# Kernel optimization log

Hardware: AMD Instinct MI355X
Metric: run time of the kernel (lower is better)

Reference implementation:

```python
import jax, jax.numpy as jnp
import numpy as np
import math

D = 768; H = 8; HD = D // H; T = 1024; V = 32000; M = 10
BLOCK = 128          # flex-attention block size (sliding_window_num_blocks granularity)
TAU = 1.0            # gumbel_temp
MAXC = 10            # max middle-block visits == scan length
EPS = 1e-6
IFP = 0.95           # initial_forward_prob

def rms(x):
    return x * jax.lax.rsqrt(jnp.mean(x * x, axis=-1, keepdims=True) + EPS)

def make_rope(t):
    # Rotary.__init__: dim//4 real inv freqs + dim//4 zeros -> cos/sin of shape [t, HD//2]
    inv = (1.0 / 1024) ** jnp.linspace(0.0, 1.0, HD // 4)
    inv = jnp.concatenate([inv, jnp.zeros(HD // 4)])
    th = jnp.arange(t, dtype=jnp.float32)[:, None] * inv[None, :]
    return jnp.cos(th), jnp.sin(th)

def rope(x, cos, sin):
    # x: [1,T,H,HD]
    c = cos[None, :, None, :]; s = sin[None, :, None, :]
    x1, x2 = jnp.split(x, 2, axis=-1)
    return jnp.concatenate([x1 * c + x2 * s, -x1 * s + x2 * c], axis=-1)

def attn(x, ve, wq, wk, wv, wo, lam, cos, sin, mask):
    q = (x @ wq.T).reshape(1, T, H, HD)
    k = (x @ wk.T).reshape(1, T, H, HD)
    v = (x @ wv.T).reshape(1, T, H, HD)
    if ve is not None:
        v = lam[0] * v + lam[1] * ve.reshape(1, T, H, HD)
    else:
        v = lam[0] * v
    q = rope(rms(q), cos, sin); k = rope(rms(k), cos, sin)
    sc = jnp.einsum('bthd,bshd->bhts', q, k) * (1.0 / math.sqrt(HD))
    sc = jnp.where(mask, sc, -1e30)
    y = jnp.einsum('bhts,bshd->bthd', jax.nn.softmax(sc, axis=-1), v).reshape(1, T, D)
    return y @ wo.T

def mlp(x, fc, pr):
    return jnp.square(jax.nn.relu(x @ fc.T)) @ pr.T

def fwd(tokens, embed_w, ve_w, lm_head_w,
        in_wq, in_wk, in_wv, in_wo, in_attn_lam, in_fc, in_pr, in_lam,
        mid_wq, mid_wk, mid_wv, mid_wo, mid_attn_lam, mid_fc, mid_pr, router_w, router_b,
        out_wq, out_wk, out_wv, out_wo, out_attn_lam, out_fc, out_pr, out_lam,
        gumbel_u, window_blocks, max_block_count):
    cos, sin = make_rope(T)
    qi = jnp.arange(T)
    mask = ((qi[:, None] >= qi[None, :]) &
            ((qi[:, None] // BLOCK - qi[None, :] // BLOCK) < window_blocks))[None, None]
    x = rms(embed_w[tokens][None])     # norm(embed(inputs))
    x0 = x
    ve = ve_w[tokens][None]            # X=1 value embedding, reused for output block
    # ---- input FixedBlock ----
    h = in_lam[0] * x + in_lam[1] * x0
    h = h + attn(rms(h), ve, in_wq, in_wk, in_wv, in_wo, in_attn_lam, cos, sin, mask)
    h = h + mlp(rms(h), in_fc, in_pr)
    # ---- middle routing loop (fixed-length scan, masked once exited) ----
    g = -jnp.log(-jnp.log(gumbel_u + 1e-10) + 1e-10)  # [MAXC, M+1] gumbel noise
    mbc = jnp.float32(max_block_count)
    def step(carry, gi):
        x, cur, done, cnt = carry
        y = x + attn(rms(x), None, mid_wq[cur], mid_wk[cur], mid_wv[cur], mid_wo[cur],
                     mid_attn_lam[cur], cos, sin, mask)
        y = y + mlp(rms(y), mid_fc[cur], mid_pr[cur])
        feat = jnp.concatenate([y.mean(axis=1), jnp.stack([cnt, mbc])[None]], axis=-1)  # [1, D+2]
        logits = feat @ router_w[cur].T + router_b[cur]                                  # [1, M+1]
        route = jax.nn.softmax((logits + gi[None]) / TAU, axis=-1)
        nxt = jnp.argmax(route[0]).astype(jnp.int32)
        new_cnt = cnt + 1.0
        exit_now = (nxt == M) | (new_cnt >= mbc)
        x = jnp.where(done, x, y)
        cnt = jnp.where(done, cnt, new_cnt)
        new_done = done | exit_now
        cur = jnp.where(new_done, cur, nxt)
        return (x, cur, new_done, cnt), None
    init = (h, jnp.int32(0), jnp.bool_(False), jnp.float32(0.0))
    (x, _, _, _), _ = jax.lax.scan(step, init, g)
    # ---- output FixedBlock ----
    y = out_lam[0] * x + out_lam[1] * x0
    y = y + attn(rms(y), ve, out_wq, out_wk, out_wv, out_wo, out_attn_lam, cos, sin, mask)
    y = y + mlp(rms(y), out_fc, out_pr)
    logits = rms(y) @ lm_head_w.T
    return 30.0 * jnp.tanh(logits / 30.0)

def setup_inputs() -> dict:
    key = jax.random.key(0)
    ks = iter(jax.random.split(key, 64))
    def w(*s, std=0.02):
        return (std * jax.random.normal(next(ks), s)).astype(jnp.float32)
    rb = np.full((M, M + 1), math.log((1.0 - IFP) / M), dtype=np.float32)
    for i in range(M):
        rb[i, min(i + 1, M)] = math.log(IFP)
    inp = {
        'tokens': jax.random.randint(next(ks), (T,), 0, V, dtype=jnp.int32),
        'embed_w': w(V, D), 've_w': w(V, D), 'lm_head_w': w(V, D),
        'in_wq': w(D, D), 'in_wk': w(D, D), 'in_wv': w(D, D), 'in_wo': w(D, D),
        'in_attn_lam': jnp.array([0.5, 0.5], jnp.float32),
        'in_fc': w(4 * D, D), 'in_pr': w(D, 4 * D),
        'in_lam': jnp.array([1.0, 0.0], jnp.float32),
        'mid_wq': w(M, D, D), 'mid_wk': w(M, D, D), 'mid_wv': w(M, D, D), 'mid_wo': w(M, D, D),
        'mid_attn_lam': jnp.tile(jnp.array([0.5, 0.5], jnp.float32), (M, 1)),
        'mid_fc': w(M, 4 * D, D), 'mid_pr': w(M, D, 4 * D),
        'router_w': w(M, M + 1, D + 2, std=0.001),
        'router_b': jnp.asarray(rb),
        'out_wq': w(D, D), 'out_wk': w(D, D), 'out_wv': w(D, D), 'out_wo': w(D, D),
        'out_attn_lam': jnp.array([0.5, 0.5], jnp.float32),
        'out_fc': w(4 * D, D), 'out_pr': w(D, 4 * D),
        'out_lam': jnp.array([1.0, 0.0], jnp.float32),
        'gumbel_u': jax.random.uniform(next(ks), (MAXC, M + 1), dtype=jnp.float32),
        'window_blocks': 4,
        'max_block_count': MAXC,
    }
    return inp

def reference(tokens, embed_w, ve_w, lm_head_w,
              in_wq, in_wk, in_wv, in_wo, in_attn_lam, in_fc, in_pr, in_lam,
              mid_wq, mid_wk, mid_wv, mid_wo, mid_attn_lam, mid_fc, mid_pr, router_w, router_b,
              out_wq, out_wk, out_wv, out_wo, out_attn_lam, out_fc, out_pr, out_lam,
              gumbel_u, window_blocks, max_block_count):
    return fwd(tokens, embed_w, ve_w, lm_head_w,
               in_wq, in_wk, in_wv, in_wo, in_attn_lam, in_fc, in_pr, in_lam,
               mid_wq, mid_wk, mid_wv, mid_wo, mid_attn_lam, mid_fc, mid_pr, router_w, router_b,
               out_wq, out_wk, out_wv, out_wo, out_attn_lam, out_fc, out_pr, out_lam,
               gumbel_u, window_blocks, max_block_count)
```

## Files before the change

### kernel.cpp

```cpp
#include <hip/hip_runtime.h>
#include <hip/hip_bf16.h>

namespace {

constexpr int cT   = 1024;
constexpr int cD   = 768;
constexpr int cH   = 8;
constexpr int cHD  = 96;
constexpr int cM   = 10;
constexpr int cDff = 3072;
constexpr int cV   = 32000;
constexpr int cTD  = cT * cD;
constexpr float cEps = 1e-6f;

constexpr long oWQ = 0;
constexpr long oWK = 589824;
constexpr long oWV = 2L * 589824;
constexpr long oWO = 3L * 589824;
constexpr long oFC = 4L * 589824;
constexpr long oPR = 4L * 589824 + 2359296;
constexpr long cWTOT = 4L * 589824 + 2L * 2359296;

typedef __attribute__((ext_vector_type(8))) short short8;
typedef __attribute__((ext_vector_type(4))) float f32x4;

__device__ inline short bf16r(float f) {
  union { float f; unsigned u; } x{f};
  unsigned r = (x.u + 0x7FFF + ((x.u >> 16) & 1)) >> 16;
  return (short)r;
}

__device__ inline float bf2f(short s) {
  union { unsigned u; float f; } x;
  x.u = ((unsigned)(unsigned short)s) << 16;
  return x.f;
}


__global__ void init_state_k(int* cur, int* done, float* cnt) {
  if (threadIdx.x == 0) { *cur = 0; *done = 0; *cnt = 0.0f; }
}

__global__ void rope_pre_k(float* __restrict__ cosb, float* __restrict__ sinb) {
  int idx = blockIdx.x * blockDim.x + threadIdx.x;
  if (idx >= cT * 48) return;
  int t = idx / 48, j = idx % 48;
  float th = 0.0f;
  if (j < 24) th = (float)t * powf(1.0f / 1024.0f, (float)j / 23.0f);
  cosb[idx] = cosf(th);
  sinb[idx] = sinf(th);
}

__global__ __launch_bounds__(256) void embed_rms_k(const int* __restrict__ tok,
    const float* __restrict__ ew, const float* __restrict__ vw,
    float* __restrict__ x0, float* __restrict__ ve) {
  int t = blockIdx.x;
  int tk = tok[t];
  const float* er = ew + (size_t)tk * cD;
  const float* vr = vw + (size_t)tk * cD;
  __shared__ float red[256];
  float s = 0.f;
  for (int d = threadIdx.x; d < cD; d += 256) { float e = er[d]; s += e * e; }
  red[threadIdx.x] = s; __syncthreads();
  for (int st = 128; st; st >>= 1) { if (threadIdx.x < st) red[threadIdx.x] += red[threadIdx.x + st]; __syncthreads(); }
  float sc = rsqrtf(red[0] / cD + cEps);
  for (int d = threadIdx.x; d < cD; d += 256) {
    x0[(size_t)t * cD + d] = er[d] * sc;
    ve[(size_t)t * cD + d] = vr[d];
  }
}

__global__ __launch_bounds__(256) void rms_rows_bf(const float* __restrict__ in,
    short* __restrict__ out, const int* done) {
  if (done && *done) return;
  int t = blockIdx.x;
  const float* r = in + (size_t)t * cD;
  __shared__ float red[256];
  float s = 0.f;
  for (int d = threadIdx.x; d < cD; d += 256) { float v = r[d]; s += v * v; }
  red[threadIdx.x] = s; __syncthreads();
  for (int st = 128; st; st >>= 1) { if (threadIdx.x < st) red[threadIdx.x] += red[threadIdx.x + st]; __syncthreads(); }
  float sc = rsqrtf(red[0] / cD + cEps);
  short* o = out + (size_t)t * cD;
  for (int d = threadIdx.x; d < cD; d += 256) o[d] = bf16r(r[d] * sc);
}

__global__ void axpy_lam_k(const float* __restrict__ lam, const float* __restrict__ a,
                           const float* __restrict__ b, float* __restrict__ o, int n) {
  int i = blockIdx.x * 256 + threadIdx.x;
  if (i < n) o[i] = lam[0] * a[i] + lam[1] * b[i];
}


__global__ __launch_bounds__(256) void convertw_k(const float* __restrict__ s0,
    const float* __restrict__ s1, const float* __restrict__ s2, const float* __restrict__ s3,
    const float* __restrict__ s4, const float* __restrict__ s5, short* __restrict__ dst,
    const int* __restrict__ cur, const int* __restrict__ done) {
  if (done && *done) return;
  long e = ((long)blockIdx.x * 256 + threadIdx.x) * 8;
  if (e >= cWTOT) return;
  long cu = cur ? (long)(*cur) : 0L;
  const float* src;
  if (e < oWK)      src = s0 + cu * 589824  + e;
  else if (e < oWV) src = s1 + cu * 589824  + (e - oWK);
  else if (e < oWO) src = s2 + cu * 589824  + (e - oWV);
  else if (e < oFC) src = s3 + cu * 589824  + (e - oWO);
  else if (e < oPR) src = s4 + cu * 2359296 + (e - oFC);
  else              src = s5 + cu * 2359296 + (e - oPR);
  float4 a0 = *(const float4*)src;
  float4 a1 = *(const float4*)(src + 4);
  short8 sv;
  sv[0]=bf16r(a0.x); sv[1]=bf16r(a0.y); sv[2]=bf16r(a0.z); sv[3]=bf16r(a0.w);
  sv[4]=bf16r(a1.x); sv[5]=bf16r(a1.y); sv[6]=bf16r(a1.z); sv[7]=bf16r(a1.w);
  *(short8*)(dst + e) = sv;
}

__global__ __launch_bounds__(256) void conv1_k(const float* __restrict__ src,
    short* __restrict__ dst, long nchunk) {
  long i = (long)blockIdx.x * 256 + threadIdx.x;
  if (i >= nchunk) return;
  long e = i * 8;
  float4 a0 = *(const float4*)(src + e);
  float4 a1 = *(const float4*)(src + e + 4);
  short8 sv;
  sv[0]=bf16r(a0.x); sv[1]=bf16r(a0.y); sv[2]=bf16r(a0.z); sv[3]=bf16r(a0.w);
  sv[4]=bf16r(a1.x); sv[5]=bf16r(a1.y); sv[6]=bf16r(a1.z); sv[7]=bf16r(a1.w);
  *(short8*)(dst + e) = sv;
}


__global__ __launch_bounds__(256) void qkv_k(const short* __restrict__ A,
    const short* __restrict__ Wb,
    short* __restrict__ qo, short* __restrict__ ko, short* __restrict__ vo,
    const int* __restrict__ done, const float* __restrict__ lamb,
    const int* __restrict__ cur, const float* __restrict__ vep,
    const float* __restrict__ cosb, const float* __restrict__ sinb) {
  if (done && *done) return;
  const int z = blockIdx.z;
  const short* W = Wb + (long)z * 589824L;
  const int h  = blockIdx.x;
  const int bm = blockIdx.y * 64;
  __shared__ short As[2][64][40];
  __shared__ short Bs[2][96][40];
  const int tid = threadIdx.x;
  const int w = tid >> 6, lane = tid & 63;
  const int fr = lane & 15, fg = lane >> 4;
  const int ar = tid >> 2, ac2 = (tid & 3) << 3;
  const int br1 = (256 + tid) >> 2, bc1 = ((256 + tid) & 3) << 3;

  short8 aN, bN0, bN1;
  aN  = *(const short8*)(A + (size_t)(bm + ar) * cD + ac2);
  bN0 = *(const short8*)(W + (size_t)(h * cHD + ar) * cD + ac2);
  if (tid < 128) bN1 = *(const short8*)(W + (size_t)(h * cHD + br1) * cD + bc1);
  *(short8*)&As[0][ar][ac2] = aN;
  *(short8*)&Bs[0][ar][ac2] = bN0;
  if (tid < 128) *(short8*)&Bs[0][br1][bc1] = bN1;
  __syncthreads();

  f32x4 acc[6] = {};
  int cb = 0;
  for (int kt = 0; kt < cD; kt += 32) {
    const int ktn = kt + 32;
    const bool hn = ktn < cD;
    if (hn) {
      aN  = *(const short8*)(A + (size_t)(bm + ar) * cD + ktn + ac2);
      bN0 = *(const short8*)(W + (size_t)(h * cHD + ar) * cD + ktn + ac2);
      if (tid < 128) bN1 = *(const short8*)(W + (size_t)(h * cHD + br1) * cD + ktn + bc1);
    }
    short8 af = *(const short8*)&As[cb][w * 16 + fr][fg * 8];
#pragma unroll
    for (int n = 0; n < 6; ++n) {
      short8 bf = *(const short8*)&Bs[cb][n * 16 + fr][fg * 8];
      acc[n] = __builtin_amdgcn_mfma_f32_16x16x32_bf16(af, bf, acc[n], 0, 0, 0);
    }
    if (hn) {
      *(short8*)&As[cb ^ 1][ar][ac2] = aN;
      *(short8*)&Bs[cb ^ 1][ar][ac2] = bN0;
      if (tid < 128) *(short8*)&Bs[cb ^ 1][br1][bc1] = bN1;
    }
    __syncthreads();
    cb ^= 1;
  }

  const int t0 = bm + w * 16 + fg * 4;
  if (z < 2) {
    float scl[4];
#pragma unroll
    for (int r = 0; r < 4; ++r) {
      float s = 0.f;
#pragma unroll
      for (int n = 0; n < 6; ++n) s += acc[n][r] * acc[n][r];
#pragma unroll
      for (int mm = 1; mm < 16; mm <<= 1) s += __shfl_xor(s, mm, 64);
      scl[r] = rsqrtf(s * (1.0f / 96.0f) + cEps);
    }
    short* C = (z == 0 ? qo : ko);
#pragma unroll
    for (int r = 0; r < 4; ++r) {
      int t = t0 + r;
      short* orow = C + (size_t)t * cD + h * cHD;
#pragma unroll
      for (int n = 0; n < 3; ++n) {
        int j = n * 16 + fr;
        float c = cosb[t * 48 + j], sn = sinb[t * 48 + j];
        float x1 = acc[n][r] * scl[r], x2 = acc[n + 3][r] * scl[r];
        orow[j]      = bf16r(x1 * c + x2 * sn);
        orow[j + 48] = bf16r(-x1 * sn + x2 * c);
      }
    }
  } else {
    int cu = cur ? *cur : 0;
    float l0 = lamb[2 * cu], l1 = lamb[2 * cu + 1];
#pragma unroll
    for (int r = 0; r < 4; ++r) {
      int t = t0 + r;
#pragma unroll
      for (int n = 0; n < 6; ++n) {
        float val = l0 * acc[n][r];
        if (vep) val += l1 * vep[(size_t)t * cD + h * cHD + n * 16 + fr];
        vo[(size_t)t * cD + h * cHD + n * 16 + fr] = bf16r(val);
      }
    }
  }
}


__global__ __launch_bounds__(256) void attn_f(const short* __restrict__ q,
    const short* __restrict__ k, const short* __restrict__ v, short* __restrict__ o,
    const int* __restrict__ wbp, const int* done) {
  if (done && *done) return;
  const int qb = blockIdx.x;
  const int h  = blockIdx.y;
  const int q0 = qb * 64;
  const int qb128 = q0 >> 7;
  const int wb = *wbp;
  int kb_lo = qb128 - wb + 1; if (kb_lo < 0) kb_lo = 0;

  __shared__ short Ksh[128][136];
  __shared__ short Vt[96][136];

  const int tid  = threadIdx.x;
  const int w    = tid >> 6;
  const int lane = tid & 63;
  const int fr   = lane & 15;
  const int fg   = lane >> 4;

  short8 qf[3];
  {
    const short* qrow = q + (size_t)(q0 + w * 16 + fr) * cD + h * cHD;
#pragma unroll
    for (int ks = 0; ks < 3; ++ks) qf[ks] = *(const short8*)(qrow + ks * 32 + fg * 8);
  }

  f32x4 accO[6] = {};
  float mrun[4], lrun[4];
#pragma unroll
  for (int r = 0; r < 4; ++r) { mrun[r] = -1e30f; lrun[r] = 0.f; }

  for (int kb = kb_lo; kb <= qb128; ++kb) {
    __syncthreads();
    const int key0 = kb * 128;
#pragma unroll
    for (int c = 0; c < 6; ++c) {
      int idx = c * 256 + tid;
      int row = idx / 12, colc = (idx % 12) * 8;
      *(short8*)&Ksh[row][colc] =
          *(const short8*)(k + (size_t)(key0 + row) * cD + h * cHD + colc);
      short8 vv = *(const short8*)(v + (size_t)(key0 + row) * cD + h * cHD + colc);
#pragma unroll
      for (int i = 0; i < 8; ++i) Vt[colc + i][row] = vv[i];
    }
    __syncthreads();

    f32x4 s[8];
#pragma unroll
    for (int n = 0; n < 8; ++n) s[n] = (f32x4){0.f, 0.f, 0.f, 0.f};
#pragma unroll
    for (int ks = 0; ks < 3; ++ks) {
#pragma unroll
      for (int n = 0; n < 8; ++n) {
        short8 kf = *(const short8*)&Ksh[n * 16 + fr][ks * 32 + fg * 8];
        s[n] = __builtin_amdgcn_mfma_f32_16x16x32_bf16(qf[ks], kf, s[n], 0, 0, 0);
      }
    }

    float pmax[4] = {-1e30f, -1e30f, -1e30f, -1e30f};
#pragma unroll
    for (int n = 0; n < 8; ++n)
#pragma unroll
      for (int r = 0; r < 4; ++r) {
        float val = s[n][r] * 0.10206207261596577f;
        int key  = key0 + n * 16 + fr;
        int qrow = q0 + w * 16 + fg * 4 + r;
        if (key > qrow) val = -1e30f;
        s[n][r] = val;
        pmax[r] = fmaxf(pmax[r], val);
      }
#pragma unroll
    for (int mm = 1; mm < 16; mm <<= 1)
#pragma unroll
      for (int r = 0; r < 4; ++r) pmax[r] = fmaxf(pmax[r], __shfl_xor(pmax[r], mm, 64));
    float alpha[4], psum[4];
#pragma unroll
    for (int r = 0; r < 4; ++r) {
      float mn = fmaxf(mrun[r], pmax[r]);
      alpha[r] = __expf(mrun[r] - mn);
      mrun[r] = mn;
      psum[r] = 0.f;
    }
#pragma unroll
    for (int n = 0; n < 8; ++n)
#pragma unroll
      for (int r = 0; r < 4; ++r) {
        float p = __expf(s[n][r] - mrun[r]);
        s[n][r] = p;
        psum[r] += p;
      }
#pragma unroll
    for (int mm = 1; mm < 16; mm <<= 1)
#pragma unroll
      for (int r = 0; r < 4; ++r) psum[r] += __shfl_xor(psum[r], mm, 64);
#pragma unroll
    for (int r = 0; r < 4; ++r) lrun[r] = lrun[r] * alpha[r] + psum[r];
#pragma unroll
    for (int n = 0; n < 6; ++n) {
      f32x4 t = accO[n];
#pragma unroll
      for (int r = 0; r < 4; ++r) t[r] *= alpha[r];
      accO[n] = t;
    }

    __syncthreads();
#pragma unroll
    for (int n = 0; n < 8; ++n)
#pragma unroll
      for (int r = 0; r < 4; ++r)
        Ksh[w * 16 + fg * 4 + r][n * 16 + fr] = bf16r(s[n][r]);
    __syncthreads();

#pragma unroll
    for (int ks = 0; ks < 4; ++ks) {
      short8 pf = *(const short8*)&Ksh[w * 16 + fr][ks * 32 + fg * 8];
#pragma unroll
      for (int n = 0; n < 6; ++n) {
        short8 vf = *(const short8*)&Vt[n * 16 + fr][ks * 32 + fg * 8];
        accO[n] = __builtin_amdgcn_mfma_f32_16x16x32_bf16(pf, vf, accO[n], 0, 0, 0);
      }
    }
  }

#pragma unroll
  for (int r = 0; r < 4; ++r) {
    float inv = 1.0f / lrun[r];
    int t = q0 + w * 16 + fg * 4 + r;
#pragma unroll
    for (int n = 0; n < 6; ++n)
      o[(size_t)t * cD + h * cHD + n * 16 + fr] = bf16r(accO[n][r] * inv);
  }
}


template <int EPI, typename OT>
__global__ __launch_bounds__(256) void gemm64_k(const short* __restrict__ A,
    const short* __restrict__ W, OT* __restrict__ C, const int* __restrict__ done,
    const float* __restrict__ res, int ld, int kn, int N) {
  if (done && *done) return;
  const int bm = blockIdx.y * 64;
  const int bn = blockIdx.x * 64;
  const int k0 = blockIdx.z * kn;
  __shared__ short As[2][64][40];
  __shared__ short Bs[2][64][40];
  const int tid = threadIdx.x;
  const int wid = tid >> 6, lane = tid & 63;
  const int wr = wid >> 1, wc = wid & 1;
  const int fr = lane & 15, fg = lane >> 4;
  const int ar = tid >> 2, ac = (tid & 3) << 3;

  short8 aN = *(const short8*)(A + (size_t)(bm + ar) * ld + k0 + ac);
  short8 bN = *(const short8*)(W + (size_t)(bn + ar) * ld + k0 + ac);
  *(short8*)&As[0][ar][ac] = aN;
  *(short8*)&Bs[0][ar][ac] = bN;
  __syncthreads();

  f32x4 acc[2][2] = {};
  int cb = 0;
  for (int kt = 0; kt < kn; kt += 32) {
    const int ktn = kt + 32;
    const bool hn = ktn < kn;
    if (hn) {
      aN = *(const short8*)(A + (size_t)(bm + ar) * ld + k0 + ktn + ac);
      bN = *(const short8*)(W + (size_t)(bn + ar) * ld + k0 + ktn + ac);
    }
    short8 af[2], bfv[2];
#pragma unroll
    for (int m = 0; m < 2; ++m) af[m] = *(const short8*)&As[cb][wr * 32 + m * 16 + fr][fg * 8];
#pragma unroll
    for (int n = 0; n < 2; ++n) bfv[n] = *(const short8*)&Bs[cb][wc * 32 + n * 16 + fr][fg * 8];
#pragma unroll
    for (int m = 0; m < 2; ++m)
#pragma unroll
      for (int n = 0; n < 2; ++n)
        acc[m][n] = __builtin_amdgcn_mfma_f32_16x16x32_bf16(af[m], bfv[n], acc[m][n], 0, 0, 0);
    if (hn) {
      *(short8*)&As[cb ^ 1][ar][ac] = aN;
      *(short8*)&Bs[cb ^ 1][ar][ac] = bN;
    }
    __syncthreads();
    cb ^= 1;
  }
#pragma unroll
  for (int m = 0; m < 2; ++m)
#pragma unroll
    for (int n = 0; n < 2; ++n)
#pragma unroll
      for (int r = 0; r < 4; ++r) {
        int row = bm + wr * 32 + m * 16 + fg * 4 + r;
        int col = bn + wc * 32 + n * 16 + fr;
        float val = acc[m][n][r];
        if (EPI == 1) {
          val += res[(size_t)row * N + col];
          C[(size_t)row * N + col] = val;
        } else {
          C[(size_t)blockIdx.z * cTD + (size_t)row * N + col] = (OT)bf16r(val);
        }
      }
}


__global__ __launch_bounds__(256) void reduce_k(const short* __restrict__ pb,
    float* __restrict__ y, float* __restrict__ x, float* __restrict__ feat,
    const int* done) {
  if (done && *done) return;
  __shared__ float red[256];
  const int d = blockIdx.x * 32 + (threadIdx.x & 31);
  const int tc = threadIdx.x >> 5;
  float s = 0.f;
  for (int t = tc * 128; t < tc * 128 + 128; ++t) {
    size_t i = (size_t)t * cD + d;
    float v = y[i];
#pragma unroll
    for (int z = 0; z < 4; ++z) v += bf2f(pb[(size_t)z * cTD + i]);
    y[i] = v;
    if (x) x[i] = v;
    s += v;
  }
  if (feat) {
    red[threadIdx.x] = s; __syncthreads();
    if (threadIdx.x < 32) {
      float tot = 0.f;
#pragma unroll
      for (int c = 0; c < 8; ++c) tot += red[c * 32 + threadIdx.x];
      feat[d] = tot * (1.0f / cT);
    }
  }
}


__global__ __launch_bounds__(256) void mgemm_fc_k(const short* __restrict__ A,
    const short* __restrict__ W, short* __restrict__ C, const int* __restrict__ done,
    int K, int N) {
  if (done && *done) return;
  const int bm = blockIdx.y * 64;
  const int bn = blockIdx.x * 128;
  __shared__ short As[2][64][40];
  __shared__ short Bs[2][128][40];
  const int tid = threadIdx.x;
  const int wid = tid >> 6, lane = tid & 63;
  const int wr = wid >> 1, wc = wid & 1;
  const int fr = lane & 15, fg = lane >> 4;
  const int ar = tid >> 2, ac = (tid & 3) << 3;
  const int br1 = (256 + tid) >> 2, bc1 = ((256 + tid) & 3) << 3;

  short8 aN, bN0, bN1;
  aN  = *(const short8*)(A + (size_t)(bm + ar) * K + ac);
  bN0 = *(const short8*)(W + (size_t)(bn + ar) * K + ac);
  bN1 = *(const short8*)(W + (size_t)(bn + br1) * K + bc1);
  *(short8*)&As[0][ar][ac] = aN;
  *(short8*)&Bs[0][ar][ac] = bN0;
  *(short8*)&Bs[0][br1][bc1] = bN1;
  __syncthreads();

  f32x4 acc[2][4] = {};
  int cb = 0;
  for (int kt = 0; kt < K; kt += 32) {
    const int ktn = kt + 32;
    const bool hn = ktn < K;
    if (hn) {
      aN  = *(const short8*)(A + (size_t)(bm + ar) * K + ktn + ac);
      bN0 = *(const short8*)(W + (size_t)(bn + ar) * K + ktn + ac);
      bN1 = *(const short8*)(W + (size_t)(bn + br1) * K + ktn + bc1);
    }
    short8 af[2], bfv[4];
#pragma unroll
    for (int m = 0; m < 2; ++m) af[m] = *(const short8*)&As[cb][wr * 32 + m * 16 + fr][fg * 8];
#pragma unroll
    for (int n = 0; n < 4; ++n) bfv[n] = *(const short8*)&Bs[cb][wc * 64 + n * 16 + fr][fg * 8];
#pragma unroll
    for (int m = 0; m < 2; ++m)
#pragma unroll
      for (int n = 0; n < 4; ++n)
        acc[m][n] = __builtin_amdgcn_mfma_f32_16x16x32_bf16(af[m], bfv[n], acc[m][n], 0, 0, 0);
    if (hn) {
      *(short8*)&As[cb ^ 1][ar][ac] = aN;
      *(short8*)&Bs[cb ^ 1][ar][ac] = bN0;
      *(short8*)&Bs[cb ^ 1][br1][bc1] = bN1;
    }
    __syncthreads();
    cb ^= 1;
  }
#pragma unroll
  for (int m = 0; m < 2; ++m)
#pragma unroll
    for (int n = 0; n < 4; ++n)
#pragma unroll
      for (int r = 0; r < 4; ++r) {
        int row = bm + wr * 32 + m * 16 + fg * 4 + r;
        int col = bn + wc * 64 + n * 16 + fr;
        float val = acc[m][n][r];
        val = fmaxf(val, 0.f); val = val * val;
        C[(size_t)row * N + col] = bf16r(val);
      }
}


__global__ __launch_bounds__(512) void gemm_lm_k(const short* __restrict__ A,
    const short* __restrict__ W, float* __restrict__ C) {
  const int nwg = (cV / 128) * (cT / 256);
  const int cpx = nwg / 8;
  const int swz = (blockIdx.x % 8) * cpx + blockIdx.x / 8;
  const int bm = (swz % 4) * 256;
  const int bn = (swz / 4) * 128;
  __shared__ short As[2][256][40];
  __shared__ short Bs[2][128][40];
  const int tid = threadIdx.x;
  const int wid = tid >> 6, lane = tid & 63;
  const int wr = wid >> 1, wc = wid & 1;
  const int fr = lane & 15, fg = lane >> 4;
  const int ar0 = tid >> 2, ac0 = (tid & 3) << 3;
  const int ar1 = (512 + tid) >> 2, ac1 = ((512 + tid) & 3) << 3;

  short8 aN0, aN1, bN;
  aN0 = *(const short8*)(A + (size_t)(bm + ar0) * cD + ac0);
  aN1 = *(const short8*)(A + (size_t)(bm + ar1) * cD + ac1);
  bN  = *(const short8*)(W + (size_t)(bn + ar0) * cD + ac0);
  *(short8*)&As[0][ar0][ac0] = aN0;
  *(short8*)&As[0][ar1][ac1] = aN1;
  *(short8*)&Bs[0][ar0][ac0] = bN;
  __syncthreads();

  f32x4 acc[4][4] = {};
  int cb = 0;
  for (int kt = 0; kt < cD; kt += 32) {
    const int ktn = kt + 32;
    const bool hn = ktn < cD;
    if (hn) {
      aN0 = *(const short8*)(A + (size_t)(bm + ar0) * cD + ktn + ac0);
      aN1 = *(const short8*)(A + (size_t)(bm + ar1) * cD + ktn + ac1);
      bN  = *(const short8*)(W + (size_t)(bn + ar0) * cD + ktn + ac0);
    }
    short8 af[4], bfv[4];
#pragma unroll
    for (int m = 0; m < 4; ++m) af[m] = *(const short8*)&As[cb][wr * 64 + m * 16 + fr][fg * 8];
#pragma unroll
    for (int n = 0; n < 4; ++n) bfv[n] = *(const short8*)&Bs[cb][wc * 64 + n * 16 + fr][fg * 8];
#pragma unroll
    for (int m = 0; m < 4; ++m)
#pragma unroll
      for (int n = 0; n < 4; ++n)
        acc[m][n] = __builtin_amdgcn_mfma_f32_16x16x32_bf16(af[m], bfv[n], acc[m][n], 0, 0, 0);
    if (hn) {
      *(short8*)&As[cb ^ 1][ar0][ac0] = aN0;
      *(short8*)&As[cb ^ 1][ar1][ac1] = aN1;
      *(short8*)&Bs[cb ^ 1][ar0][ac0] = bN;
    }
    __syncthreads();
    cb ^= 1;
  }
#pragma unroll
  for (int m = 0; m < 4; ++m)
#pragma unroll
    for (int n = 0; n < 4; ++n)
#pragma unroll
      for (int r = 0; r < 4; ++r) {
        int row = bm + wr * 64 + m * 16 + fg * 4 + r;
        int col = bn + wc * 64 + n * 16 + fr;
        C[(size_t)row * cV + col] = 30.f * tanhf(acc[m][n][r] * (1.f / 30.f));
      }
}


__global__ void router_step_k(const float* __restrict__ feat, const float* __restrict__ rw,
    const float* __restrict__ rb, const float* __restrict__ gu, int iter,
    const int* __restrict__ mbcp, int* cur, int* done, float* cnt) {
  if (*done) return;
  __shared__ float lg[cM + 1];
  const int tid = threadIdx.x;
  const int c = *cur;
  const float mbc = (float)(*mbcp);
  const float cn = *cnt;
  for (int j = 0; j < cM + 1; ++j) {
    const float* w = rw + ((size_t)c * (cM + 1) + j) * (cD + 2);
    float s = 0.f;
    for (int d = tid; d < cD; d += 64) s += feat[d] * w[d];
#pragma unroll
    for (int mm = 32; mm; mm >>= 1) s += __shfl_xor(s, mm, 64);
    if (tid == 0) {
      s += cn * w[cD] + mbc * w[cD + 1] + rb[c * (cM + 1) + j];
      float u = gu[iter * (cM + 1) + j];
      float inner = -logf(u + 1e-10f) + 1e-10f;
      lg[j] = s - logf(inner);
    }
  }
  __syncthreads();
  if (tid == 0) {
    int nxt = 0; float best = lg[0];
    for (int j = 1; j < cM + 1; ++j) if (lg[j] > best) { best = lg[j]; nxt = j; }
    float nc = cn + 1.0f;
    int ex = (nxt == cM) || (nc >= mbc);
    *cnt = nc;
    if (ex) *done = 1; else *cur = nxt;
  }
}

}


extern "C" void kernel_launch(void* const* d_in, const int* in_sizes, int n_in,
                              void* d_out, int out_size, void* d_ws, size_t ws_size,
                              hipStream_t stream) {
  const int*   tokens    = (const int*)d_in[0];
  const float* embed_w   = (const float*)d_in[1];
  const float* ve_w      = (const float*)d_in[2];
  const float* lm_head_w = (const float*)d_in[3];
  const float* in_wq  = (const float*)d_in[4];
  const float* in_wk  = (const float*)d_in[5];
  const float* in_wv  = (const float*)d_in[6];
  const float* in_wo  = (const float*)d_in[7];
  const float* in_al  = (const float*)d_in[8];
  const float* in_fc  = (const float*)d_in[9];
  const float* in_pr  = (const float*)d_in[10];
  const float* in_lam = (const float*)d_in[11];
  const float* mid_wq = (const float*)d_in[12];
  const float* mid_wk = (const float*)d_in[13];
  const float* mid_wv = (const float*)d_in[14];
  const float* mid_wo = (const float*)d_in[15];
  const float* mid_al = (const float*)d_in[16];
  const float* mid_fc = (const float*)d_in[17];
  const float* mid_pr = (const float*)d_in[18];
  const float* router_w = (const float*)d_in[19];
  const float* router_b = (const float*)d_in[20];
  const float* out_wq = (const float*)d_in[21];
  const float* out_wk = (const float*)d_in[22];
  const float* out_wv = (const float*)d_in[23];
  const float* out_wo = (const float*)d_in[24];
  const float* out_al = (const float*)d_in[25];
  const float* out_fc = (const float*)d_in[26];
  const float* out_pr = (const float*)d_in[27];
  const float* out_lam = (const float*)d_in[28];
  const float* gumbel_u = (const float*)d_in[29];
  const int*   wbp  = (const int*)d_in[30];
  const int*   mbcp = (const int*)d_in[31];
  float* outp = (float*)d_out;

  float* ws = (float*)d_ws;
  float* xb   = ws;
  float* x0b  = xb  + cTD;
  float* veb  = x0b + cTD;
  float* yb   = veb + cTD;
  float* cosb = yb  + cTD;
  float* sinb = cosb + cT * 48;
  float* feat = sinb + cT * 48;
  int*   curp  = (int*)(feat + 784);
  int*   donep = curp + 1;
  float* cntp  = (float*)(curp + 2);
  short* xnbf  = (short*)(feat + 784 + 4);
  short* aobf  = xnbf + cTD;
  short* qbf   = aobf + cTD;
  short* kbf   = qbf  + cTD;
  short* vbf   = kbf  + cTD;
  short* pbuf  = aobf;
  short* hidbf = vbf  + cTD;
  short* wbf   = hidbf + (size_t)cT * cDff;

  const dim3 gQKV(cH, cT / 64, 3);
  const dim3 gWO(cD / 64, cT / 64, 1);
  const dim3 gPR(cD / 64, cT / 64, 4);
  const dim3 gFF(cDff / 128, cT / 64, 1);
  const dim3 gLM(1000, 1, 1);
  const dim3 gAttn(cT / 64, cH, 1);
  const int gRed = cD / 32;
  const int gConvW = (int)(cWTOT / 8 / 256);
  const long lmChunks = (long)cV * cD / 8;
  const int gConvLM = (int)(lmChunks / 256);

  auto layer = [&](const float* wq, const float* wk, const float* wv, const float* wo,
                   const float* alam, const float* fc, const float* pr,
                   const int* cur, const int* done,
                   float* xin, float* yout, const float* vept,
                   float* xcom, float* featp) {
    convertw_k<<<gConvW, 256, 0, stream>>>(wq, wk, wv, wo, fc, pr, wbf, cur, done);
    rms_rows_bf<<<cT, 256, 0, stream>>>(xin, xnbf, done);
    qkv_k<<<gQKV, 256, 0, stream>>>(xnbf, wbf, qbf, kbf, vbf, done, alam, cur, vept,
                                    cosb, sinb);
    attn_f<<<gAttn, 256, 0, stream>>>(qbf, kbf, vbf, aobf, wbp, done);
    gemm64_k<1, float><<<gWO, 256, 0, stream>>>(aobf, wbf + oWO, yout, done, xin,
                                                cD, cD, cD);
    rms_rows_bf<<<cT, 256, 0, stream>>>(yout, xnbf, done);
    mgemm_fc_k<<<gFF, 256, 0, stream>>>(xnbf, wbf + oFC, hidbf, done, cD, cDff);
    gemm64_k<4, short><<<gPR, 256, 0, stream>>>(hidbf, wbf + oPR, pbuf, done, nullptr,
                                                cDff, cDff / 4, cD);
    reduce_k<<<gRed, 256, 0, stream>>>(pbuf, yout, xcom, featp, done);
  };

  init_state_k<<<1, 64, 0, stream>>>(curp, donep, cntp);
  rope_pre_k<<<(cT * 48 + 255) / 256, 256, 0, stream>>>(cosb, sinb);
  embed_rms_k<<<cT, 256, 0, stream>>>(tokens, embed_w, ve_w, x0b, veb);

  axpy_lam_k<<<cTD / 256, 256, 0, stream>>>(in_lam, x0b, x0b, xb, cTD);
  layer(in_wq, in_wk, in_wv, in_wo, in_al, in_fc, in_pr, nullptr, nullptr,
        xb, xb, veb, nullptr, nullptr);

  for (int it = 0; it < cM; ++it) {
    layer(mid_wq, mid_wk, mid_wv, mid_wo, mid_al, mid_fc, mid_pr,
          curp, donep, xb, yb, nullptr, xb, feat);
    router_step_k<<<1, 64, 0, stream>>>(feat, router_w, router_b, gumbel_u, it, mbcp,
                                        curp, donep, cntp);
  }

  axpy_lam_k<<<cTD / 256, 256, 0, stream>>>(out_lam, xb, x0b, xb, cTD);
  layer(out_wq, out_wk, out_wv, out_wo, out_al, out_fc, out_pr, nullptr, nullptr,
        xb, xb, veb, nullptr, nullptr);

  conv1_k<<<gConvLM, 256, 0, stream>>>(lm_head_w, wbf, lmChunks);
  rms_rows_bf<<<cT, 256, 0, stream>>>(xb, xnbf, nullptr);
  gemm_lm_k<<<gLM, 512, 0, stream>>>(xnbf, wbf, outp);
}
```

Before: 2.637 ms.

## Fuse weight conversion with RMSNorm and fold MLP RMSNorm into GEMM epilogue/prologue

Merges the per-layer weight conversion and the input RMSNorm into one launch, which also zeroes a per-row sum-of-squares buffer. The Wo GEMM epilogue now accumulates each row's squared residual output via shuffles and atomics. The FC GEMM reads fp32 activations directly and applies the RMS scale while converting to bf16. This removes two launches per layer and the separate normalized-activation round trip through memory. The cost is atomics in the Wo epilogue and twice-as-wide fp32 A loads in the FC GEMM.

```diff
diff --git a/kernel.cpp b/kernel.cpp
--- a/kernel.cpp
+++ b/kernel.cpp
@@ -20,6 +20,7 @@
 constexpr long oFC = 4L * 589824;
 constexpr long oPR = 4L * 589824 + 2359296;
 constexpr long cWTOT = 4L * 589824 + 2L * 2359296;
+constexpr int cConvBlocks = (int)(cWTOT / 8 / 256);
 
 typedef __attribute__((ext_vector_type(8))) short short8;
 typedef __attribute__((ext_vector_type(4))) float f32x4;
@@ -92,27 +93,42 @@
 }
 
 
-__global__ __launch_bounds__(256) void convertw_k(const float* __restrict__ s0,
+__global__ __launch_bounds__(256) void layer_pre_k(const float* __restrict__ s0,
     const float* __restrict__ s1, const float* __restrict__ s2, const float* __restrict__ s3,
     const float* __restrict__ s4, const float* __restrict__ s5, short* __restrict__ dst,
-    const int* __restrict__ cur, const int* __restrict__ done) {
+    const int* __restrict__ cur, const int* __restrict__ done,
+    const float* __restrict__ xin, short* __restrict__ xnbf, float* __restrict__ rsum) {
   if (done && *done) return;
-  long e = ((long)blockIdx.x * 256 + threadIdx.x) * 8;
-  if (e >= cWTOT) return;
-  long cu = cur ? (long)(*cur) : 0L;
-  const float* src;
-  if (e < oWK)      src = s0 + cu * 589824  + e;
-  else if (e < oWV) src = s1 + cu * 589824  + (e - oWK);
-  else if (e < oWO) src = s2 + cu * 589824  + (e - oWV);
-  else if (e < oFC) src = s3 + cu * 589824  + (e - oWO);
-  else if (e < oPR) src = s4 + cu * 2359296 + (e - oFC);
-  else              src = s5 + cu * 2359296 + (e - oPR);
-  float4 a0 = *(const float4*)src;
-  float4 a1 = *(const float4*)(src + 4);
-  short8 sv;
-  sv[0]=bf16r(a0.x); sv[1]=bf16r(a0.y); sv[2]=bf16r(a0.z); sv[3]=bf16r(a0.w);
-  sv[4]=bf16r(a1.x); sv[5]=bf16r(a1.y); sv[6]=bf16r(a1.z); sv[7]=bf16r(a1.w);
-  *(short8*)(dst + e) = sv;
+  const int b = blockIdx.x;
+  if (b < cConvBlocks) {
+    long e = ((long)b * 256 + threadIdx.x) * 8;
+    long cu = cur ? (long)(*cur) : 0L;
+    const float* src;
+    if (e < oWK)      src = s0 + cu * 589824  + e;
+    else if (e < oWV) src = s1 + cu * 589824  + (e - oWK);
+    else if (e < oWO) src = s2 + cu * 589824  + (e - oWV);
+    else if (e < oFC) src = s3 + cu * 589824  + (e - oWO);
+    else if (e < oPR) src = s4 + cu * 2359296 + (e - oFC);
+    else              src = s5 + cu * 2359296 + (e - oPR);
+    float4 a0 = *(const float4*)src;
+    float4 a1 = *(const float4*)(src + 4);
+    short8 sv;
+    sv[0]=bf16r(a0.x); sv[1]=bf16r(a0.y); sv[2]=bf16r(a0.z); sv[3]=bf16r(a0.w);
+    sv[4]=bf16r(a1.x); sv[5]=bf16r(a1.y); sv[6]=bf16r(a1.z); sv[7]=bf16r(a1.w);
+    *(short8*)(dst + e) = sv;
+  } else {
+    const int t = b - cConvBlocks;
+    const float* r = xin + (size_t)t * cD;
+    __shared__ float red[256];
+    float s = 0.f;
+    for (int d = threadIdx.x; d < cD; d += 256) { float v = r[d]; s += v * v; }
+    red[threadIdx.x] = s; __syncthreads();
+    for (int st = 128; st; st >>= 1) { if (threadIdx.x < st) red[threadIdx.x] += red[threadIdx.x + st]; __syncthreads(); }
+    float sc = rsqrtf(red[0] / cD + cEps);
+    short* o = xnbf + (size_t)t * cD;
+    for (int d = threadIdx.x; d < cD; d += 256) o[d] = bf16r(r[d] * sc);
+    if (threadIdx.x == 0) rsum[t] = 0.f;
+  }
 }
 
 __global__ __launch_bounds__(256) void conv1_k(const float* __restrict__ src,
@@ -363,7 +379,7 @@
 template <int EPI, typename OT>
 __global__ __launch_bounds__(256) void gemm64_k(const short* __restrict__ A,
     const short* __restrict__ W, OT* __restrict__ C, const int* __restrict__ done,
-    const float* __restrict__ res, int ld, int kn, int N) {
+    const float* __restrict__ res, float* __restrict__ rsum, int ld, int kn, int N) {
   if (done && *done) return;
   const int bm = blockIdx.y * 64;
   const int bn = blockIdx.x * 64;
@@ -411,18 +427,105 @@
 #pragma unroll
   for (int m = 0; m < 2; ++m)
 #pragma unroll
-    for (int n = 0; n < 2; ++n)
-#pragma unroll
-      for (int r = 0; r < 4; ++r) {
-        int row = bm + wr * 32 + m * 16 + fg * 4 + r;
-        int col = bn + wc * 32 + n * 16 + fr;
+    for (int r = 0; r < 4; ++r) {
+      const int row = bm + wr * 32 + m * 16 + fg * 4 + r;
+      float p = 0.f;
+#pragma unroll
+      for (int n = 0; n < 2; ++n) {
+        const int col = bn + wc * 32 + n * 16 + fr;
         float val = acc[m][n][r];
-        if (EPI == 1) {
+        if constexpr (EPI == 1) {
           val += res[(size_t)row * N + col];
           C[(size_t)row * N + col] = val;
+          p += val * val;
         } else {
           C[(size_t)blockIdx.z * cTD + (size_t)row * N + col] = (OT)bf16r(val);
         }
+      }
+      if constexpr (EPI == 1) {
+#pragma unroll
+        for (int mm = 1; mm < 16; mm <<= 1) p += __shfl_xor(p, mm, 64);
+        if (fr == 0) atomicAdd(&rsum[row], p);
+      }
+    }
+}
+
+
+__global__ __launch_bounds__(256) void mgemm_fc_k(const float* __restrict__ Ay,
+    const float* __restrict__ rsum, const short* __restrict__ W, short* __restrict__ C,
+    const int* __restrict__ done, int K, int N) {
+  if (done && *done) return;
+  const int bm = blockIdx.y * 64;
+  const int bn = blockIdx.x * 128;
+  __shared__ short As[2][64][40];
+  __shared__ short Bs[2][128][40];
+  const int tid = threadIdx.x;
+  const int wid = tid >> 6, lane = tid & 63;
+  const int wr = wid >> 1, wc = wid & 1;
+  const int fr = lane & 15, fg = lane >> 4;
+  const int ar = tid >> 2, ac = (tid & 3) << 3;
+  const int br1 = (256 + tid) >> 2, bc1 = ((256 + tid) & 3) << 3;
+
+  const float ascl = rsqrtf(rsum[bm + ar] * (1.0f / cD) + cEps);
+  const float* arow = Ay + (size_t)(bm + ar) * K;
+
+  auto loadA = [&](int kt) -> short8 {
+    float4 a0 = *(const float4*)(arow + kt + ac);
+    float4 a1 = *(const float4*)(arow + kt + ac + 4);
+    short8 sv;
+    sv[0]=bf16r(a0.x*ascl); sv[1]=bf16r(a0.y*ascl); sv[2]=bf16r(a0.z*ascl); sv[3]=bf16r(a0.w*ascl);
+    sv[4]=bf16r(a1.x*ascl); sv[5]=bf16r(a1.y*ascl); sv[6]=bf16r(a1.z*ascl); sv[7]=bf16r(a1.w*ascl);
+    return sv;
+  };
+
+  short8 aN, bN0, bN1;
+  aN  = loadA(0);
+  bN0 = *(const short8*)(W + (size_t)(bn + ar) * K + ac);
+  bN1 = *(const short8*)(W + (size_t)(bn + br1) * K + bc1);
+  *(short8*)&As[0][ar][ac] = aN;
+  *(short8*)&Bs[0][ar][ac] = bN0;
+  *(short8*)&Bs[0][br1][bc1] = bN1;
+  __syncthreads();
+
+  f32x4 acc[2][4] = {};
+  int cb = 0;
+  for (int kt = 0; kt < K; kt += 32) {
+    const int ktn = kt + 32;
+    const bool hn = ktn < K;
+    if (hn) {
+      aN  = loadA(ktn);
+      bN0 = *(const short8*)(W + (size_t)(bn + ar) * K + ktn + ac);
+      bN1 = *(const short8*)(W + (size_t)(bn + br1) * K + ktn + bc1);
+    }
+    short8 af[2], bfv[4];
+#pragma unroll
+    for (int m = 0; m < 2; ++m) af[m] = *(const short8*)&As[cb][wr * 32 + m * 16 + fr][fg * 8];
+#pragma unroll
+    for (int n = 0; n < 4; ++n) bfv[n] = *(const short8*)&Bs[cb][wc * 64 + n * 16 + fr][fg * 8];
+#pragma unroll
+    for (int m = 0; m < 2; ++m)
+#pragma unroll
+      for (int n = 0; n < 4; ++n)
+        acc[m][n] = __builtin_amdgcn_mfma_f32_16x16x32_bf16(af[m], bfv[n], acc[m][n], 0, 0, 0);
+    if (hn) {
+      *(short8*)&As[cb ^ 1][ar][ac] = aN;
+      *(short8*)&Bs[cb ^ 1][ar][ac] = bN0;
+      *(short8*)&Bs[cb ^ 1][br1][bc1] = bN1;
+    }
+    __syncthreads();
+    cb ^= 1;
+  }
+#pragma unroll
+  for (int m = 0; m < 2; ++m)
+#pragma unroll
+    for (int n = 0; n < 4; ++n)
+#pragma unroll
+      for (int r = 0; r < 4; ++r) {
+        int row = bm + wr * 32 + m * 16 + fg * 4 + r;
+        int col = bn + wc * 64 + n * 16 + fr;
+        float val = acc[m][n][r];
+        val = fmaxf(val, 0.f); val = val * val;
+        C[(size_t)row * N + col] = bf16r(val);
       }
 }
 
@@ -456,70 +559,37 @@
 }
 
 
-__global__ __launch_bounds__(256) void mgemm_fc_k(const short* __restrict__ A,
-    const short* __restrict__ W, short* __restrict__ C, const int* __restrict__ done,
-    int K, int N) {
-  if (done && *done) return;
-  const int bm = blockIdx.y * 64;
-  const int bn = blockIdx.x * 128;
-  __shared__ short As[2][64][40];
-  __shared__ short Bs[2][128][40];
+__global__ void router_step_k(const float* __restrict__ feat, const float* __restrict__ rw,
+    const float* __restrict__ rb, const float* __restrict__ gu, int iter,
+    const int* __restrict__ mbcp, int* cur, int* done, float* cnt) {
+  if (*done) return;
+  __shared__ float lg[cM + 1];
   const int tid = threadIdx.x;
-  const int wid = tid >> 6, lane = tid & 63;
-  const int wr = wid >> 1, wc = wid & 1;
-  const int fr = lane & 15, fg = lane >> 4;
-  const int ar = tid >> 2, ac = (tid & 3) << 3;
-  const int br1 = (256 + tid) >> 2, bc1 = ((256 + tid) & 3) << 3;
-
-  short8 aN, bN0, bN1;
-  aN  = *(const short8*)(A + (size_t)(bm + ar) * K + ac);
-  bN0 = *(const short8*)(W + (size_t)(bn + ar) * K + ac);
-  bN1 = *(const short8*)(W + (size_t)(bn + br1) * K + bc1);
-  *(short8*)&As[0][ar][ac] = aN;
-  *(short8*)&Bs[0][ar][ac] = bN0;
-  *(short8*)&Bs[0][br1][bc1] = bN1;
+  const int c = *cur;
+  const float mbc = (float)(*mbcp);
+  const float cn = *cnt;
+  for (int j = 0; j < cM + 1; ++j) {
+    const float* w = rw + ((size_t)c * (cM + 1) + j) * (cD + 2);
+    float s = 0.f;
+    for (int d = tid; d < cD; d += 64) s += feat[d] * w[d];
+#pragma unroll
+    for (int mm = 32; mm; mm >>= 1) s += __shfl_xor(s, mm, 64);
+    if (tid == 0) {
+      s += cn * w[cD] + mbc * w[cD + 1] + rb[c * (cM + 1) + j];
+      float u = gu[iter * (cM + 1) + j];
+      float inner = -logf(u + 1e-10f) + 1e-10f;
+      lg[j] = s - logf(inner);
+    }
+  }
   __syncthreads();
-
-  f32x4 acc[2][4] = {};
-  int cb = 0;
-  for (int kt = 0; kt < K; kt += 32) {
-    const int ktn = kt + 32;
-    const bool hn = ktn < K;
-    if (hn) {
-      aN  = *(const short8*)(A + (size_t)(bm + ar) * K + ktn + ac);
-      bN0 = *(const short8*)(W + (size_t)(bn + ar) * K + ktn + ac);
-      bN1 = *(const short8*)(W + (size_t)(bn + br1) * K + ktn + bc1);
-    }
-    short8 af[2], bfv[4];
-#pragma unroll
-    for (int m = 0; m < 2; ++m) af[m] = *(const short8*)&As[cb][wr * 32 + m * 16 + fr][fg * 8];
-#pragma unroll
-    for (int n = 0; n < 4; ++n) bfv[n] = *(const short8*)&Bs[cb][wc * 64 + n * 16 + fr][fg * 8];
-#pragma unroll
-    for (int m = 0; m < 2; ++m)
-#pragma unroll
-      for (int n = 0; n < 4; ++n)
-        acc[m][n] = __builtin_amdgcn_mfma_f32_16x16x32_bf16(af[m], bfv[n], acc[m][n], 0, 0, 0);
-    if (hn) {
-      *(short8*)&As[cb ^ 1][ar][ac] = aN;
-      *(short8*)&Bs[cb ^ 1][ar][ac] = bN0;
-      *(short8*)&Bs[cb ^ 1][br1][bc1] = bN1;
-    }
-    __syncthreads();
-    cb ^= 1;
-  }
-#pragma unroll
-  for (int m = 0; m < 2; ++m)
-#pragma unroll
-    for (int n = 0; n < 4; ++n)
-#pragma unroll
-      for (int r = 0; r < 4; ++r) {
-        int row = bm + wr * 32 + m * 16 + fg * 4 + r;
-        int col = bn + wc * 64 + n * 16 + fr;
-        float val = acc[m][n][r];
-        val = fmaxf(val, 0.f); val = val * val;
-        C[(size_t)row * N + col] = bf16r(val);
-      }
+  if (tid == 0) {
+    int nxt = 0; float best = lg[0];
+    for (int j = 1; j < cM + 1; ++j) if (lg[j] > best) { best = lg[j]; nxt = j; }
+    float nc = cn + 1.0f;
+    int ex = (nxt == cM) || (nc >= mbc);
+    *cnt = nc;
+    if (ex) *done = 1; else *cur = nxt;
+  }
 }
 
 
@@ -586,40 +656,6 @@
         int col = bn + wc * 64 + n * 16 + fr;
         C[(size_t)row * cV + col] = 30.f * tanhf(acc[m][n][r] * (1.f / 30.f));
       }
-}
-
-
-__global__ void router_step_k(const float* __restrict__ feat, const float* __restrict__ rw,
-    const float* __restrict__ rb, const float* __restrict__ gu, int iter,
-    const int* __restrict__ mbcp, int* cur, int* done, float* cnt) {
-  if (*done) return;
-  __shared__ float lg[cM + 1];
-  const int tid = threadIdx.x;
-  const int c = *cur;
-  const float mbc = (float)(*mbcp);
-  const float cn = *cnt;
-  for (int j = 0; j < cM + 1; ++j) {
-    const float* w = rw + ((size_t)c * (cM + 1) + j) * (cD + 2);
-    float s = 0.f;
-    for (int d = tid; d < cD; d += 64) s += feat[d] * w[d];
-#pragma unroll
-    for (int mm = 32; mm; mm >>= 1) s += __shfl_xor(s, mm, 64);
-    if (tid == 0) {
-      s += cn * w[cD] + mbc * w[cD + 1] + rb[c * (cM + 1) + j];
-      float u = gu[iter * (cM + 1) + j];
-      float inner = -logf(u + 1e-10f) + 1e-10f;
-      lg[j] = s - logf(inner);
-    }
-  }
-  __syncthreads();
-  if (tid == 0) {
-    int nxt = 0; float best = lg[0];
-    for (int j = 1; j < cM + 1; ++j) if (lg[j] > best) { best = lg[j]; nxt = j; }
-    float nc = cn + 1.0f;
-    int ex = (nxt == cM) || (nc >= mbc);
-    *cnt = nc;
-    if (ex) *done = 1; else *cur = nxt;
-  }
 }
 
 }
@@ -669,11 +705,12 @@
   float* yb   = veb + cTD;
   float* cosb = yb  + cTD;
   float* sinb = cosb + cT * 48;
-  float* feat = sinb + cT * 48;
+  float* rsum = sinb + cT * 48;
+  float* feat = rsum + 1024;
   int*   curp  = (int*)(feat + 784);
   int*   donep = curp + 1;
   float* cntp  = (float*)(curp + 2);
-  short* xnbf  = (short*)(feat + 784 + 4);
+  short* xnbf  = (short*)(feat + 784 + 8);
   short* aobf  = xnbf + cTD;
   short* qbf   = aobf + cTD;
   short* kbf   = qbf  + cTD;
@@ -682,6 +719,7 @@
   short* hidbf = vbf  + cTD;
   short* wbf   = hidbf + (size_t)cT * cDff;
 
+  const dim3 gPre(cConvBlocks + cT, 1, 1);
   const dim3 gQKV(cH, cT / 64, 3);
   const dim3 gWO(cD / 64, cT / 64, 1);
   const dim3 gPR(cD / 64, cT / 64, 4);
@@ -689,7 +727,6 @@
   const dim3 gLM(1000, 1, 1);
   const dim3 gAttn(cT / 64, cH, 1);
   const int gRed = cD / 32;
-  const int gConvW = (int)(cWTOT / 8 / 256);
   const long lmChunks = (long)cV * cD / 8;
   const int gConvLM = (int)(lmChunks / 256);
 
@@ -698,17 +735,16 @@
                    const int* cur, const int* done,
                    float* xin, float* yout, const float* vept,
                    float* xcom, float* featp) {
-    convertw_k<<<gConvW, 256, 0, stream>>>(wq, wk, wv, wo, fc, pr, wbf, cur, done);
-    rms_rows_bf<<<cT, 256, 0, stream>>>(xin, xnbf, done);
+    layer_pre_k<<<gPre, 256, 0, stream>>>(wq, wk, wv, wo, fc, pr, wbf, cur, done,
+                                          xin, xnbf, rsum);
     qkv_k<<<gQKV, 256, 0, stream>>>(xnbf, wbf, qbf, kbf, vbf, done, alam, cur, vept,
                                     cosb, sinb);
     attn_f<<<gAttn, 256, 0, stream>>>(qbf, kbf, vbf, aobf, wbp, done);
-    gemm64_k<1, float><<<gWO, 256, 0, stream>>>(aobf, wbf + oWO, yout, done, xin,
+    gemm64_k<1, float><<<gWO, 256, 0, stream>>>(aobf, wbf + oWO, yout, done, xin, rsum,
                                                 cD, cD, cD);
-    rms_rows_bf<<<cT, 256, 0, stream>>>(yout, xnbf, done);
-    mgemm_fc_k<<<gFF, 256, 0, stream>>>(xnbf, wbf + oFC, hidbf, done, cD, cDff);
+    mgemm_fc_k<<<gFF, 256, 0, stream>>>(yout, rsum, wbf + oFC, hidbf, done, cD, cDff);
     gemm64_k<4, short><<<gPR, 256, 0, stream>>>(hidbf, wbf + oPR, pbuf, done, nullptr,
-                                                cDff, cDff / 4, cD);
+                                                nullptr, cDff, cDff / 4, cD);
     reduce_k<<<gRed, 256, 0, stream>>>(pbuf, yout, xcom, featp, done);
   };
 
```

New measurement: 2.631 ms. No clear change (-0.2%).
